# Kernel tuning notes

Hardware: AMD Instinct MI355X
Metric: run time of the kernel (lower is better)

## Reference

```python
import jax, jax.numpy as jnp
import numpy as np

TEMP = 0.07
POS_WINDOW = 2
EPS = 1e-8
NEG = -1e9  # finite large-negative for masking (safe under vjp)


def _l2norm(x):
    # matches F.normalize(dim=-1) with eps=1e-12
    n = jnp.sqrt(jnp.sum(x * x, axis=-1, keepdims=True))
    return x / jnp.maximum(n, 1e-12)


def setup_inputs() -> dict:
    key = jax.random.key(0)
    k1, k2, k3, k4, k5 = jax.random.split(key, 5)
    B, T, D = 32, 1024, 256
    eeg_enc = jax.random.normal(k1, (B, T, D), dtype=jnp.float32)
    eye_enc = jax.random.normal(k2, (B, T, D), dtype=jnp.float32)
    mask = jax.random.randint(k3, (B, T), 0, 2, dtype=jnp.int32)
    W_eeg = jax.random.normal(k4, (D, D), dtype=jnp.float32) / np.sqrt(D)
    W_eye = jax.random.normal(k5, (D, D), dtype=jnp.float32) / np.sqrt(D)
    return {"eeg_enc": eeg_enc, "eye_enc": eye_enc, "mask": mask,
            "W_eeg": W_eeg, "W_eye": W_eye}


def reference(eeg_enc, eye_enc, mask, W_eeg, W_eye):
    B, T, D = eeg_enc.shape
    valid = mask > 0  # (B,T)
    # nn.Linear(bias=False): x @ W.T, then L2-normalize
    e = _l2norm(jnp.einsum('btd,ed->bte', eeg_enc, W_eeg))
    v = _l2norm(jnp.einsum('btd,ed->bte', eye_enc, W_eye))
    sims = jnp.einsum('bid,bjd->bij', e, v) / TEMP  # (B,T,T)
    # rank of each valid step within the compressed (gathered) ordering
    rank = jnp.cumsum(valid.astype(jnp.int32), axis=-1) - 1  # (B,T)
    band = jnp.abs(rank[:, :, None] - rank[:, None, :]) <= POS_WINDOW
    pair = valid[:, :, None] & valid[:, None, :]  # both steps valid
    pos = pair & band
    # per-row max over positive (banded) entries
    pos_scores = jnp.max(jnp.where(pos, sims, NEG), axis=-1)  # (B,T)
    # logsumexp over valid columns (the gathered sims row)
    lse = jax.nn.logsumexp(jnp.where(valid[:, None, :], sims, NEG), axis=-1)
    row_loss = -(pos_scores - lse)  # (B,T)
    Tv = jnp.sum(valid, axis=-1)  # (B,)
    per_b = jnp.sum(jnp.where(valid, row_loss, 0.0), axis=-1) / jnp.maximum(Tv, 1)
    per_b = jnp.where(Tv >= 2, per_b, 0.0)  # skip samples with <2 valid steps
    return jnp.sum(per_b) / (B + EPS)
```

## Files before the change

### kernel.cpp

```cpp
#include <hip/hip_runtime.h>
#include <hip/hip_bf16.h>

typedef __attribute__((ext_vector_type(8))) short bf16x8;
typedef __attribute__((ext_vector_type(4))) float f32x4;

#define INVT (1.0f/0.07f)

static __device__ __forceinline__ short f2bf(float f){
    unsigned int u = __float_as_uint(f);
    unsigned int r = (u + 0x7fffu + ((u >> 16) & 1u)) >> 16;
    return (short)r;
}
static __device__ __forceinline__ float bf2f(short s){
    return __uint_as_float(((unsigned int)(unsigned short)s) << 16);
}

static __device__ __forceinline__ void gld16(const void* g, void* l){
    __builtin_amdgcn_global_load_lds(
        (const __attribute__((address_space(1))) unsigned int*)g,
        (__attribute__((address_space(3))) unsigned int*)l, 16, 0, 0);
}

__global__ __launch_bounds__(256) void prep_kernel(const float* __restrict__ Weeg,
                                                   const float* __restrict__ Weye,
                                                   const int* __restrict__ mask,
                                                   short* __restrict__ Wout,
                                                   int* __restrict__ rank,
                                                   int* __restrict__ idx,
                                                   int* __restrict__ Tv,
                                                   float* __restrict__ cb,
                                                   float* __restrict__ bsum){
    __shared__ int ssum[256];
    int tid = threadIdx.x;
    if (blockIdx.x < 512){
        int i = blockIdx.x * 256 + tid;
        float v = (i < 65536) ? Weeg[i] : Weye[i - 65536];
        Wout[i] = f2bf(v);
        return;
    }
    int b = blockIdx.x - 512;
    if (tid == 0) bsum[b] = 0.f;
    int local[4]; int s = 0;
    #pragma unroll
    for (int q = 0; q < 4; ++q){
        int t = tid*4 + q;
        local[q] = (mask[b*1024 + t] > 0) ? 1 : 0;
        s += local[q];
    }
    ssum[tid] = s;
    __syncthreads();
    for (int off = 1; off < 256; off <<= 1){
        int add = (tid >= off) ? ssum[tid - off] : 0;
        __syncthreads();
        ssum[tid] += add;
        __syncthreads();
    }
    int run = ssum[tid] - s;
    #pragma unroll
    for (int q = 0; q < 4; ++q){
        int t = tid*4 + q;
        int g = b*1024 + t;
        run += local[q];
        rank[g] = run - 1;
        cb[g]   = local[q] ? 0.0f : -1e9f;
        if (local[q]) idx[b*1024 + run - 1] = t;
    }
    if (tid == 255) Tv[b] = ssum[255];
}

__global__ __launch_bounds__(256, 2) void proj_kernel(const float* __restrict__ Aeeg,
                                                      const float* __restrict__ Aeye,
                                                      const short* __restrict__ Wbf,
                                                      short* __restrict__ Eout,
                                                      short* __restrict__ Vout){
    __shared__ short sW[2][64 * 256];
    int sel = blockIdx.y;
    const float* A   = sel ? Aeye : Aeeg;
    const short* W   = Wbf + sel * 65536;
    short*       Out = sel ? Vout : Eout;

    int tid = threadIdx.x;
    int w = tid >> 6, lane = tid & 63;
    int l15 = lane & 15, lq = lane >> 4;
    int kb  = lq * 8;
    int row0 = blockIdx.x * 64;

    int ro   = lane >> 5;
    int cs   = lane & 31;
    int s7   = l15 & 7;

    #pragma unroll
    for (int p = 0; p < 8; ++p){
        int rr = (p*2 + ro) & 7;
        gld16(W + (size_t)(w*16 + p*2 + ro)*256 + (cs ^ rr)*8,
              &sW[0][(w*16 + p*2) * 256]);
    }
    #pragma unroll
    for (int p = 0; p < 8; ++p){
        int rr = (p*2 + ro) & 7;
        gld16(W + (size_t)(64 + w*16 + p*2 + ro)*256 + (cs ^ rr)*8,
              &sW[1][(w*16 + p*2) * 256]);
    }

    bf16x8 xf[8];
    {
        const float* ap = A + (size_t)(row0 + w*16 + l15) * 256 + kb;
        #pragma unroll
        for (int g = 0; g < 8; ++g){
            float4 x0 = *(const float4*)(ap + g*32);
            float4 x1 = *(const float4*)(ap + g*32 + 4);
            bf16x8 t;
            t[0]=f2bf(x0.x); t[1]=f2bf(x0.y); t[2]=f2bf(x0.z); t[3]=f2bf(x0.w);
            t[4]=f2bf(x1.x); t[5]=f2bf(x1.y); t[6]=f2bf(x1.z); t[7]=f2bf(x1.w);
            xf[g] = t;
        }
    }

    f32x4 acc[16];
    #pragma unroll
    for (int q = 0; q < 16; ++q) acc[q] = (f32x4){0.f,0.f,0.f,0.f};

    __syncthreads();

    #pragma unroll
    for (int nt = 0; nt < 4; ++nt){
        f32x4 c = acc[nt];
        int rbase = (nt*16 + l15) * 256;
        #pragma unroll
        for (int g = 0; g < 8; ++g){
            bf16x8 wf = *(const bf16x8*)&sW[0][rbase + (((g*4 + lq) ^ s7) << 3)];
            c = __builtin_amdgcn_mfma_f32_16x16x32_bf16(wf, xf[g], c, 0, 0, 0);
        }
        acc[nt] = c;
    }

    __syncthreads();

    #pragma unroll
    for (int p = 0; p < 8; ++p){
        int rr = (p*2 + ro) & 7;
        gld16(W + (size_t)(128 + w*16 + p*2 + ro)*256 + (cs ^ rr)*8,
              &sW[0][(w*16 + p*2) * 256]);
    }
    #pragma unroll
    for (int nt = 0; nt < 4; ++nt){
        f32x4 c = acc[4 + nt];
        int rbase = (nt*16 + l15) * 256;
        #pragma unroll
        for (int g = 0; g < 8; ++g){
            bf16x8 wf = *(const bf16x8*)&sW[1][rbase + (((g*4 + lq) ^ s7) << 3)];
            c = __builtin_amdgcn_mfma_f32_16x16x32_bf16(wf, xf[g], c, 0, 0, 0);
        }
        acc[4 + nt] = c;
    }

    __syncthreads();

    #pragma unroll
    for (int p = 0; p < 8; ++p){
        int rr = (p*2 + ro) & 7;
        gld16(W + (size_t)(192 + w*16 + p*2 + ro)*256 + (cs ^ rr)*8,
              &sW[1][(w*16 + p*2) * 256]);
    }
    #pragma unroll
    for (int nt = 0; nt < 4; ++nt){
        f32x4 c = acc[8 + nt];
        int rbase = (nt*16 + l15) * 256;
        #pragma unroll
        for (int g = 0; g < 8; ++g){
            bf16x8 wf = *(const bf16x8*)&sW[0][rbase + (((g*4 + lq) ^ s7) << 3)];
            c = __builtin_amdgcn_mfma_f32_16x16x32_bf16(wf, xf[g], c, 0, 0, 0);
        }
        acc[8 + nt] = c;
    }

    __syncthreads();

    #pragma unroll
    for (int nt = 0; nt < 4; ++nt){
        f32x4 c = acc[12 + nt];
        int rbase = (nt*16 + l15) * 256;
        #pragma unroll
        for (int g = 0; g < 8; ++g){
            bf16x8 wf = *(const bf16x8*)&sW[1][rbase + (((g*4 + lq) ^ s7) << 3)];
            c = __builtin_amdgcn_mfma_f32_16x16x32_bf16(wf, xf[g], c, 0, 0, 0);
        }
        acc[12 + nt] = c;
    }

    float ss = 0.f;
    #pragma unroll
    for (int q = 0; q < 16; ++q){
        #pragma unroll
        for (int r = 0; r < 4; ++r){ float x = acc[q][r]; ss += x*x; }
    }
    ss += __shfl_xor(ss, 16);
    ss += __shfl_xor(ss, 32);
    float scale = 1.0f / fmaxf(sqrtf(ss), 1e-12f);

    short* twrow = &sW[0][(w*16 + l15) * 256];
    #pragma unroll
    for (int q = 0; q < 16; ++q){
        short4 pk;
        pk.x = f2bf(acc[q][0] * scale);
        pk.y = f2bf(acc[q][1] * scale);
        pk.z = f2bf(acc[q][2] * scale);
        pk.w = f2bf(acc[q][3] * scale);
        int c    = (q >> 2) * 64 + (q & 3) * 16 + lq*4;
        int blk  = (c >> 3) ^ s7;
        *(short4*)(twrow + blk*8 + (c & 7)) = pk;
    }
    short* op = Out + (size_t)(row0 + w*16) * 256;
    #pragma unroll
    for (int p = 0; p < 8; ++p){
        int rloc = p*2 + (lane >> 5);
        int gblk = lane & 31;
        const short* tr = &sW[0][(w*16 + rloc) * 256 + ((gblk ^ (rloc & 7)) * 8)];
        *(int4*)(op + rloc*256 + gblk*8) = *(const int4*)tr;
    }
}

__global__ __launch_bounds__(64) void loss_kernel(const short* __restrict__ E,
                                                  const short* __restrict__ V,
                                                  const float* __restrict__ cb,
                                                  float* __restrict__ psum){
    int n  = blockIdx.x;
    int b  = (((n >> 3) & 3) << 3) | (n & 7);
    int r2 = n >> 5;
    int it = r2 & 15;
    int jh = r2 >> 4;

    int lane = threadIdx.x;
    int l15 = lane & 15, lq = lane >> 4;

    bf16x8 af[4][8];
    {
        const short* ep = E + ((size_t)b*1024 + it*64 + l15) * 256 + lq*8;
        #pragma unroll
        for (int s = 0; s < 4; ++s)
            #pragma unroll
            for (int g = 0; g < 8; ++g)
                af[s][g] = *(const bf16x8*)(ep + s*16*256 + g*32);
    }

    const short* vp  = V  + ((size_t)b*1024 + jh*512 + l15) * 256 + lq*8;
    const float* cbp = cb + b*1024 + jh*512 + l15;

    float ls[4][4];
    #pragma unroll
    for (int s = 0; s < 4; ++s)
        #pragma unroll
        for (int r = 0; r < 4; ++r) ls[s][r] = 0.f;

    bf16x8 ba[8], bb[8];
    #pragma unroll
    for (int g = 0; g < 8; ++g) ba[g] = *(const bf16x8*)(vp + g*32);
    float ca = cbp[0];
    float cbv;

    #pragma unroll 1
    for (int t = 0; t < 16; ++t){
        {
            const short* v1 = vp + (size_t)(2*t + 1) * 16 * 256;
            #pragma unroll
            for (int g = 0; g < 8; ++g) bb[g] = *(const bf16x8*)(v1 + g*32);
            cbv = cbp[(2*t + 1) * 16];
        }
        {
            f32x4 a0 = (f32x4){0.f,0.f,0.f,0.f};
            f32x4 a1 = (f32x4){0.f,0.f,0.f,0.f};
            f32x4 a2 = (f32x4){0.f,0.f,0.f,0.f};
            f32x4 a3 = (f32x4){0.f,0.f,0.f,0.f};
            #pragma unroll
            for (int g = 0; g < 8; ++g){
                a0 = __builtin_amdgcn_mfma_f32_16x16x32_bf16(af[0][g], ba[g], a0, 0, 0, 0);
                a1 = __builtin_amdgcn_mfma_f32_16x16x32_bf16(af[1][g], ba[g], a1, 0, 0, 0);
                a2 = __builtin_amdgcn_mfma_f32_16x16x32_bf16(af[2][g], ba[g], a2, 0, 0, 0);
                a3 = __builtin_amdgcn_mfma_f32_16x16x32_bf16(af[3][g], ba[g], a3, 0, 0, 0);
            }
            #pragma unroll
            for (int r = 0; r < 4; ++r){
                ls[0][r] += __expf(fmaf(a0[r], INVT, ca));
                ls[1][r] += __expf(fmaf(a1[r], INVT, ca));
                ls[2][r] += __expf(fmaf(a2[r], INVT, ca));
                ls[3][r] += __expf(fmaf(a3[r], INVT, ca));
            }
        }
        if (t < 15){
            const short* v2 = vp + (size_t)(2*t + 2) * 16 * 256;
            #pragma unroll
            for (int g = 0; g < 8; ++g) ba[g] = *(const bf16x8*)(v2 + g*32);
            ca = cbp[(2*t + 2) * 16];
        }
        {
            f32x4 a0 = (f32x4){0.f,0.f,0.f,0.f};
            f32x4 a1 = (f32x4){0.f,0.f,0.f,0.f};
            f32x4 a2 = (f32x4){0.f,0.f,0.f,0.f};
            f32x4 a3 = (f32x4){0.f,0.f,0.f,0.f};
            #pragma unroll
            for (int g = 0; g < 8; ++g){
                a0 = __builtin_amdgcn_mfma_f32_16x16x32_bf16(af[0][g], bb[g], a0, 0, 0, 0);
                a1 = __builtin_amdgcn_mfma_f32_16x16x32_bf16(af[1][g], bb[g], a1, 0, 0, 0);
                a2 = __builtin_amdgcn_mfma_f32_16x16x32_bf16(af[2][g], bb[g], a2, 0, 0, 0);
                a3 = __builtin_amdgcn_mfma_f32_16x16x32_bf16(af[3][g], bb[g], a3, 0, 0, 0);
            }
            #pragma unroll
            for (int r = 0; r < 4; ++r){
                ls[0][r] += __expf(fmaf(a0[r], INVT, cbv));
                ls[1][r] += __expf(fmaf(a1[r], INVT, cbv));
                ls[2][r] += __expf(fmaf(a2[r], INVT, cbv));
                ls[3][r] += __expf(fmaf(a3[r], INVT, cbv));
            }
        }
    }

    #pragma unroll
    for (int s = 0; s < 4; ++s)
        #pragma unroll
        for (int r = 0; r < 4; ++r){
            float v = ls[s][r];
            #pragma unroll
            for (int mm = 1; mm < 16; mm <<= 1)
                v += __shfl_xor(v, mm);
            ls[s][r] = v;
        }

    if (l15 == 0){
        float* pp = psum + (size_t)jh*32768 + (size_t)b*1024 + it*64;
        #pragma unroll
        for (int s = 0; s < 4; ++s)
            #pragma unroll
            for (int r = 0; r < 4; ++r)
                pp[s*16 + lq*4 + r] = ls[s][r];
    }
}

__global__ __launch_bounds__(256) void pos_kernel(const short* __restrict__ E,
                                                  const short* __restrict__ V,
                                                  const int* __restrict__ mask,
                                                  const int* __restrict__ rank,
                                                  const int* __restrict__ idx,
                                                  const int* __restrict__ Tv,
                                                  float* __restrict__ pmax){
    int tid = threadIdx.x;
    int gl  = tid & 15;
    int rf  = (blockIdx.x * 256 + tid) >> 4;
    int b   = rf >> 10;
    if (mask[rf] <= 0) return;

    int ri = rank[rf];
    int tv = Tv[b];
    int lo = ri - 2; if (lo < 0) lo = 0;
    int hi = ri + 2; if (hi > tv - 1) hi = tv - 1;

    const short* epp = E + (size_t)rf * 256 + gl * 16;
    float ev[16];
    {
        bf16x8 e0 = *(const bf16x8*)epp;
        bf16x8 e1 = *(const bf16x8*)(epp + 8);
        #pragma unroll
        for (int k = 0; k < 8; ++k){ ev[k] = bf2f(e0[k]); ev[8+k] = bf2f(e1[k]); }
    }
    float pm = -1e30f;
    for (int r = lo; r <= hi; ++r){
        int j = idx[b*1024 + r];
        const short* vpp = V + ((size_t)(b*1024) + j) * 256 + gl * 16;
        bf16x8 v0 = *(const bf16x8*)vpp;
        bf16x8 v1 = *(const bf16x8*)(vpp + 8);
        float s = 0.f;
        #pragma unroll
        for (int k = 0; k < 8; ++k){
            s = fmaf(ev[k],   bf2f(v0[k]), s);
            s = fmaf(ev[8+k], bf2f(v1[k]), s);
        }
        s += __shfl_xor(s, 1);
        s += __shfl_xor(s, 2);
        s += __shfl_xor(s, 4);
        s += __shfl_xor(s, 8);
        pm = fmaxf(pm, s);
    }
    if (gl == 0) pmax[rf] = pm * INVT;
}

__global__ __launch_bounds__(256) void reduce_kernel(const float* __restrict__ psum,
                                                     const float* __restrict__ pmax,
                                                     const int* __restrict__ mask,
                                                     float* __restrict__ bsum){
    int b  = blockIdx.x >> 2;
    int i  = (blockIdx.x & 3) * 256 + threadIdx.x;
    int g  = b*1024 + i;
    float a = 0.f;
    if (mask[g] > 0){
        float ps = psum[g] + psum[g + 32768];
        a = logf(ps) - pmax[g];
    }
    #pragma unroll
    for (int m = 1; m < 64; m <<= 1) a += __shfl_xor(a, m);
    if ((threadIdx.x & 63) == 0 && a != 0.f) atomicAdd(&bsum[b], a);
}

__global__ void final_kernel(const float* __restrict__ bsum,
                             const int* __restrict__ Tv,
                             float* __restrict__ out){
    int tid = threadIdx.x;
    float v = 0.f;
    if (tid < 32){
        int tv = Tv[tid];
        if (tv >= 2) v = bsum[tid] / (float)tv;
    }
    #pragma unroll
    for (int m = 1; m < 64; m <<= 1) v += __shfl_xor(v, m);
    if (tid == 0) out[0] = v / 32.0f;
}

extern "C" void kernel_launch(void* const* d_in, const int* in_sizes, int n_in,
                              void* d_out, int out_size, void* d_ws, size_t ws_size,
                              hipStream_t stream) {
    const float* eeg  = (const float*)d_in[0];
    const float* eye  = (const float*)d_in[1];
    const int*   mask = (const int*)d_in[2];
    const float* Weeg = (const float*)d_in[3];
    const float* Weye = (const float*)d_in[4];
    float* out = (float*)d_out;

    char* ws = (char*)d_ws;
    short* e_bf  = (short*)(ws);
    short* v_bf  = (short*)(ws + 16777216);
    short* wbf   = (short*)(ws + 33554432);
    int*   rank  = (int*)  (ws + 33816576);
    int*   idx   = (int*)  (ws + 33947648);
    float* cb    = (float*)(ws + 34078720);
    float* psum  = (float*)(ws + 34209792);
    float* pmax  = (float*)(ws + 34734080);
    int*   Tv    = (int*)  (ws + 34865152);
    float* bsum  = (float*)(ws + 34865280);

    prep_kernel<<<544, 256, 0, stream>>>(Weeg, Weye, mask, wbf, rank, idx, Tv, cb, bsum);
    proj_kernel<<<dim3(512, 2), 256, 0, stream>>>(eeg, eye, wbf, e_bf, v_bf);
    loss_kernel<<<1024, 64, 0, stream>>>(e_bf, v_bf, cb, psum);
    pos_kernel<<<2048, 256, 0, stream>>>(e_bf, v_bf, mask, rank, idx, Tv, pmax);
    reduce_kernel<<<128, 256, 0, stream>>>(psum, pmax, mask, bsum);
    final_kernel<<<1, 64, 0, stream>>>(bsum, Tv, out);
}
```

Baseline: 169.7 us.

## Compact valid timesteps via index gather in loss kernel to skip masked work

The logsumexp kernel now gathers E and V rows through the compacted valid-index list instead of processing all 1024×1024 entries per batch. Whole tiles beyond the valid count are skipped, and the tile is reshaped to 32 rows by 256 columns across 4 column splits. The precomputed column-bias array is dropped: masking comes from the in-tile valid count, and the reduction reads partial sums at each row's rank. This is meant to cut the matmul and exp work roughly in proportion to the masked fraction, at the cost of gathered row loads and less A-tile reuse per block.

```diff
diff --git a/kernel.cpp b/kernel.cpp
--- a/kernel.cpp
+++ b/kernel.cpp
@@ -28,7 +28,6 @@
                                                    int* __restrict__ rank,
                                                    int* __restrict__ idx,
                                                    int* __restrict__ Tv,
-                                                   float* __restrict__ cb,
                                                    float* __restrict__ bsum){
     __shared__ int ssum[256];
     int tid = threadIdx.x;
@@ -62,7 +61,6 @@
         int g = b*1024 + t;
         run += local[q];
         rank[g] = run - 1;
-        cb[g]   = local[q] ? 0.0f : -1e9f;
         if (local[q]) idx[b*1024 + run - 1] = t;
     }
     if (tid == 255) Tv[b] = ssum[255];
@@ -222,116 +220,126 @@
 
 __global__ __launch_bounds__(64) void loss_kernel(const short* __restrict__ E,
                                                   const short* __restrict__ V,
-                                                  const float* __restrict__ cb,
+                                                  const int* __restrict__ idx,
+                                                  const int* __restrict__ Tv,
                                                   float* __restrict__ psum){
     int n  = blockIdx.x;
     int b  = (((n >> 3) & 3) << 3) | (n & 7);
-    int r2 = n >> 5;
-    int it = r2 & 15;
-    int jh = r2 >> 4;
-
+    int it = (n >> 5) & 31;
+    int js = n >> 10;
+
+    int tv = Tv[b];
     int lane = threadIdx.x;
     int l15 = lane & 15, lq = lane >> 4;
 
-    bf16x8 af[4][8];
+    if (it*32 >= tv) return;
+
+    if (js*256 >= tv){
+        if (lane < 32) psum[(size_t)js*32768 + b*1024 + it*32 + lane] = 0.f;
+        return;
+    }
+
+    const int* ib = idx + b*1024;
+
+    int rA0 = it*32 + l15;
+    int rA1 = rA0 + 16;
+    int iA0 = (rA0 < tv) ? ib[rA0] : ib[0];
+    int iA1 = (rA1 < tv) ? ib[rA1] : ib[0];
+    bf16x8 af0[8], af1[8];
     {
-        const short* ep = E + ((size_t)b*1024 + it*64 + l15) * 256 + lq*8;
-        #pragma unroll
-        for (int s = 0; s < 4; ++s)
-            #pragma unroll
-            for (int g = 0; g < 8; ++g)
-                af[s][g] = *(const bf16x8*)(ep + s*16*256 + g*32);
-    }
-
-    const short* vp  = V  + ((size_t)b*1024 + jh*512 + l15) * 256 + lq*8;
-    const float* cbp = cb + b*1024 + jh*512 + l15;
-
-    float ls[4][4];
-    #pragma unroll
-    for (int s = 0; s < 4; ++s)
-        #pragma unroll
-        for (int r = 0; r < 4; ++r) ls[s][r] = 0.f;
+        const short* e0 = E + ((size_t)b*1024 + iA0)*256 + lq*8;
+        const short* e1 = E + ((size_t)b*1024 + iA1)*256 + lq*8;
+        #pragma unroll
+        for (int g = 0; g < 8; ++g){
+            af0[g] = *(const bf16x8*)(e0 + g*32);
+            af1[g] = *(const bf16x8*)(e1 + g*32);
+        }
+    }
+
+    int   iv[16];
+    float ce[16];
+    #pragma unroll
+    for (int jt = 0; jt < 16; ++jt){
+        int r  = js*256 + jt*16 + l15;
+        int ok = r < tv;
+        iv[jt] = ok ? ib[r] : ib[0];
+        ce[jt] = ok ? 0.0f : -1e9f;
+    }
+
+    const short* vb = V + (size_t)b*1024*256 + lq*8;
+
+    float ls0[4] = {0.f,0.f,0.f,0.f};
+    float ls1[4] = {0.f,0.f,0.f,0.f};
 
     bf16x8 ba[8], bb[8];
-    #pragma unroll
-    for (int g = 0; g < 8; ++g) ba[g] = *(const bf16x8*)(vp + g*32);
-    float ca = cbp[0];
-    float cbv;
-
-    #pragma unroll 1
-    for (int t = 0; t < 16; ++t){
+    {
+        const short* vp = vb + (size_t)iv[0]*256;
+        #pragma unroll
+        for (int g = 0; g < 8; ++g) ba[g] = *(const bf16x8*)(vp + g*32);
+    }
+
+    #pragma unroll
+    for (int p = 0; p < 8; ++p){
         {
-            const short* v1 = vp + (size_t)(2*t + 1) * 16 * 256;
-            #pragma unroll
-            for (int g = 0; g < 8; ++g) bb[g] = *(const bf16x8*)(v1 + g*32);
-            cbv = cbp[(2*t + 1) * 16];
+            const short* vp = vb + (size_t)iv[2*p+1]*256;
+            #pragma unroll
+            for (int g = 0; g < 8; ++g) bb[g] = *(const bf16x8*)(vp + g*32);
         }
         {
             f32x4 a0 = (f32x4){0.f,0.f,0.f,0.f};
             f32x4 a1 = (f32x4){0.f,0.f,0.f,0.f};
-            f32x4 a2 = (f32x4){0.f,0.f,0.f,0.f};
-            f32x4 a3 = (f32x4){0.f,0.f,0.f,0.f};
             #pragma unroll
             for (int g = 0; g < 8; ++g){
-                a0 = __builtin_amdgcn_mfma_f32_16x16x32_bf16(af[0][g], ba[g], a0, 0, 0, 0);
-                a1 = __builtin_amdgcn_mfma_f32_16x16x32_bf16(af[1][g], ba[g], a1, 0, 0, 0);
-                a2 = __builtin_amdgcn_mfma_f32_16x16x32_bf16(af[2][g], ba[g], a2, 0, 0, 0);
-                a3 = __builtin_amdgcn_mfma_f32_16x16x32_bf16(af[3][g], ba[g], a3, 0, 0, 0);
+                a0 = __builtin_amdgcn_mfma_f32_16x16x32_bf16(af0[g], ba[g], a0, 0, 0, 0);
+                a1 = __builtin_amdgcn_mfma_f32_16x16x32_bf16(af1[g], ba[g], a1, 0, 0, 0);
             }
+            float m = ce[2*p];
             #pragma unroll
             for (int r = 0; r < 4; ++r){
-                ls[0][r] += __expf(fmaf(a0[r], INVT, ca));
-                ls[1][r] += __expf(fmaf(a1[r], INVT, ca));
-                ls[2][r] += __expf(fmaf(a2[r], INVT, ca));
-                ls[3][r] += __expf(fmaf(a3[r], INVT, ca));
+                ls0[r] += __expf(fmaf(a0[r], INVT, m));
+                ls1[r] += __expf(fmaf(a1[r], INVT, m));
             }
         }
-        if (t < 15){
-            const short* v2 = vp + (size_t)(2*t + 2) * 16 * 256;
-            #pragma unroll
-            for (int g = 0; g < 8; ++g) ba[g] = *(const bf16x8*)(v2 + g*32);
-            ca = cbp[(2*t + 2) * 16];
+        if (p < 7){
+            const short* vp = vb + (size_t)iv[2*p+2]*256;
+            #pragma unroll
+            for (int g = 0; g < 8; ++g) ba[g] = *(const bf16x8*)(vp + g*32);
         }
         {
             f32x4 a0 = (f32x4){0.f,0.f,0.f,0.f};
             f32x4 a1 = (f32x4){0.f,0.f,0.f,0.f};
-            f32x4 a2 = (f32x4){0.f,0.f,0.f,0.f};
-            f32x4 a3 = (f32x4){0.f,0.f,0.f,0.f};
             #pragma unroll
             for (int g = 0; g < 8; ++g){
-                a0 = __builtin_amdgcn_mfma_f32_16x16x32_bf16(af[0][g], bb[g], a0, 0, 0, 0);
-                a1 = __builtin_amdgcn_mfma_f32_16x16x32_bf16(af[1][g], bb[g], a1, 0, 0, 0);
-                a2 = __builtin_amdgcn_mfma_f32_16x16x32_bf16(af[2][g], bb[g], a2, 0, 0, 0);
-                a3 = __builtin_amdgcn_mfma_f32_16x16x32_bf16(af[3][g], bb[g], a3, 0, 0, 0);
+                a0 = __builtin_amdgcn_mfma_f32_16x16x32_bf16(af0[g], bb[g], a0, 0, 0, 0);
+                a1 = __builtin_amdgcn_mfma_f32_16x16x32_bf16(af1[g], bb[g], a1, 0, 0, 0);
             }
+            float m = ce[2*p+1];
             #pragma unroll
             for (int r = 0; r < 4; ++r){
-                ls[0][r] += __expf(fmaf(a0[r], INVT, cbv));
-                ls[1][r] += __expf(fmaf(a1[r], INVT, cbv));
-                ls[2][r] += __expf(fmaf(a2[r], INVT, cbv));
-                ls[3][r] += __expf(fmaf(a3[r], INVT, cbv));
+                ls0[r] += __expf(fmaf(a0[r], INVT, m));
+                ls1[r] += __expf(fmaf(a1[r], INVT, m));
             }
         }
     }
 
     #pragma unroll
-    for (int s = 0; s < 4; ++s)
+    for (int r = 0; r < 4; ++r){
+        float v0 = ls0[r], v1 = ls1[r];
+        #pragma unroll
+        for (int mm = 1; mm < 16; mm <<= 1){
+            v0 += __shfl_xor(v0, mm);
+            v1 += __shfl_xor(v1, mm);
+        }
+        ls0[r] = v0; ls1[r] = v1;
+    }
+
+    if (l15 == 0){
+        float* pp = psum + (size_t)js*32768 + b*1024 + it*32;
         #pragma unroll
         for (int r = 0; r < 4; ++r){
-            float v = ls[s][r];
-            #pragma unroll
-            for (int mm = 1; mm < 16; mm <<= 1)
-                v += __shfl_xor(v, mm);
-            ls[s][r] = v;
-        }
-
-    if (l15 == 0){
-        float* pp = psum + (size_t)jh*32768 + (size_t)b*1024 + it*64;
-        #pragma unroll
-        for (int s = 0; s < 4; ++s)
-            #pragma unroll
-            for (int r = 0; r < 4; ++r)
-                pp[s*16 + lq*4 + r] = ls[s][r];
+            pp[lq*4 + r]      = ls0[r];
+            pp[16 + lq*4 + r] = ls1[r];
+        }
     }
 }
 
@@ -385,13 +393,15 @@
 __global__ __launch_bounds__(256) void reduce_kernel(const float* __restrict__ psum,
                                                      const float* __restrict__ pmax,
                                                      const int* __restrict__ mask,
+                                                     const int* __restrict__ rank,
                                                      float* __restrict__ bsum){
     int b  = blockIdx.x >> 2;
     int i  = (blockIdx.x & 3) * 256 + threadIdx.x;
     int g  = b*1024 + i;
     float a = 0.f;
     if (mask[g] > 0){
-        float ps = psum[g] + psum[g + 32768];
+        const float* pp = psum + b*1024 + rank[g];
+        float ps = pp[0] + pp[32768] + pp[65536] + pp[98304];
         a = logf(ps) - pmax[g];
     }
     #pragma unroll
@@ -429,16 +439,15 @@
     short* wbf   = (short*)(ws + 33554432);
     int*   rank  = (int*)  (ws + 33816576);
     int*   idx   = (int*)  (ws + 33947648);
-    float* cb    = (float*)(ws + 34078720);
     float* psum  = (float*)(ws + 34209792);
     float* pmax  = (float*)(ws + 34734080);
     int*   Tv    = (int*)  (ws + 34865152);
     float* bsum  = (float*)(ws + 34865280);
 
-    prep_kernel<<<544, 256, 0, stream>>>(Weeg, Weye, mask, wbf, rank, idx, Tv, cb, bsum);
+    prep_kernel<<<544, 256, 0, stream>>>(Weeg, Weye, mask, wbf, rank, idx, Tv, bsum);
     proj_kernel<<<dim3(512, 2), 256, 0, stream>>>(eeg, eye, wbf, e_bf, v_bf);
-    loss_kernel<<<1024, 64, 0, stream>>>(e_bf, v_bf, cb, psum);
+    loss_kernel<<<4096, 64, 0, stream>>>(e_bf, v_bf, idx, Tv, psum);
     pos_kernel<<<2048, 256, 0, stream>>>(e_bf, v_bf, mask, rank, idx, Tv, pmax);
-    reduce_kernel<<<128, 256, 0, stream>>>(psum, pmax, mask, bsum);
+    reduce_kernel<<<128, 256, 0, stream>>>(psum, pmax, mask, rank, bsum);
     final_kernel<<<1, 64, 0, stream>>>(bsum, Tv, out);
 }
```

After: 174.9 us. 3.1% more time.
